# Performance work log

Measured on AMD Instinct MI355X. Metric: run time of the kernel, lower is better.

## Reference

```python
import jax, jax.numpy as jnp
import numpy as np

EMBED_DIM = 1024
EXPAND_RATIO = 128  # head_dim; n_heads = EMBED_DIM // EXPAND_RATIO = 8
B, N = 4, 2048


def setup_inputs() -> dict:
    key = jax.random.key(0)
    ks = jax.random.split(key, 6)
    std = 0.02
    d = EMBED_DIM
    return {
        "x": jax.random.normal(ks[0], (B, N, d), dtype=jnp.float32),
        "Wq": jax.random.normal(ks[1], (d, d), dtype=jnp.float32) * std,
        "Wk": jax.random.normal(ks[2], (d, d), dtype=jnp.float32) * std,
        "Wv": jax.random.normal(ks[3], (d, d), dtype=jnp.float32) * std,
        "Wo": jax.random.normal(ks[4], (d, d), dtype=jnp.float32) * std,
        "norm_w": jnp.ones((d,), dtype=jnp.float32),
    }


def _rmsnorm(x, w, eps=1e-6):
    return x * jax.lax.rsqrt(jnp.mean(x * x, axis=-1, keepdims=True) + eps) * w


def _gla_scan(q, k, v, g):
    # q,k,v,g: [b, n, h, d]; state S: [b, h, d_k, d_v]
    b, n, h, d = q.shape
    qs, ks_, vs, gs = (jnp.moveaxis(t, 1, 0) for t in (q, k, v, g))  # [n,b,h,d]
    S0 = jnp.zeros((b, h, d, d), dtype=q.dtype)

    def step(S, inp):
        q_t, k_t, v_t, g_t = inp
        # S_t = diag(exp(g_t)) S_{t-1} + k_t^T v_t (gate on key dim)
        S = jnp.exp(g_t)[..., :, None] * S + k_t[..., :, None] * v_t[..., None, :]
        o_t = jnp.einsum('bhk,bhkv->bhv', q_t, S)
        return S, o_t

    _, outs = jax.lax.scan(step, S0, (qs, ks_, vs, gs))
    return jnp.moveaxis(outs, 0, 1)  # [b, n, h, d]


def reference(x, Wq, Wk, Wv, Wo, norm_w):
    b, n, D = x.shape
    hd = EXPAND_RATIO
    h = D // hd

    q = jax.nn.silu(x @ Wq.T)          # q_activation = silu
    f = jax.nn.sigmoid(x @ Wk.T)       # f = sigmoid(k_proj(x))
    log_f = jax.nn.log_sigmoid(f)      # faithful: logsigmoid applied to f (lower_bound=None path)
    k = 1.0 - f
    v = x @ Wv.T

    def split_heads(t):
        return t.reshape(b, n, h, hd)

    out = _gla_scan(split_heads(q), split_heads(k), split_heads(v), split_heads(log_f))
    out = out.reshape(b, n, D)
    out = _rmsnorm(out, norm_w)        # norm_pos='ogate', no output gate
    return out @ Wo.T
```

## Files before the change

kernel.cpp:

```cpp
#include <hip/hip_runtime.h>
#include <cstdint>
#include <cstddef>


typedef unsigned short u16;
using f32x4  = __attribute__((ext_vector_type(4))) float;
using bf16x8 = __attribute__((ext_vector_type(8))) short;

__device__ __forceinline__ float bf2f(u16 u) {
  union { unsigned int i; float f; } v; v.i = ((unsigned int)u) << 16; return v.f;
}
__device__ __forceinline__ u16 f2bf(float f) {
  union { float f; unsigned int i; } v; v.f = f;
  unsigned int r = v.i + 0x7fffu + ((v.i >> 16) & 1u);
  return (u16)(r >> 16);
}
__device__ __forceinline__ void async_load16(const void* g, void* l) {
  __builtin_amdgcn_global_load_lds(
      (const __attribute__((address_space(1))) unsigned int*)(uintptr_t)g,
      (__attribute__((address_space(3))) unsigned int*)(uintptr_t)l, 16, 0, 0);
}

__device__ __forceinline__ void gemm128_core(const u16* __restrict__ Ag, const u16* __restrict__ Bg,
                                             u16* smem, f32x4 (&acc)[4][4]) {
  const int tid = threadIdx.x;
  const int lane = tid & 63, wave = tid >> 6;
  const int wm = (wave & 1) * 64, wn = (wave >> 1) * 64;
  const int r = lane & 15, quad = lane >> 4;
  const int xk = r & 7;
  const u16* baseA0 = smem + (wm + r) * 64 + ((quad ^ xk) & 7) * 8;
  const u16* baseA1 = smem + (wm + r) * 64 + (((quad + 4) ^ xk) & 7) * 8;
  const u16* baseB0 = smem + 8192 + (wn + r) * 64 + ((quad ^ xk) & 7) * 8;
  const u16* baseB1 = smem + 8192 + (wn + r) * 64 + (((quad + 4) ^ xk) & 7) * 8;
  const int soff = (tid >> 3) * 1024 + (((tid & 7) ^ ((tid >> 3) & 7)) * 8);
  u16* dA = smem + wave * 512;
  u16* dB = smem + 8192 + wave * 512;
  for (int kt = 0; kt < 16; ++kt) {
    __syncthreads();
    const u16* As = Ag + kt * 64 + soff;
    const u16* Bs = Bg + kt * 64 + soff;
#pragma unroll
    for (int it = 0; it < 4; ++it) {
      async_load16(As + it * 32768, dA + it * 2048);
      async_load16(Bs + it * 32768, dB + it * 2048);
    }
    __syncthreads();
    bf16x8 af[4], bv[4];
#pragma unroll
    for (int i = 0; i < 4; ++i) af[i] = *(const bf16x8*)(baseA0 + i * 1024);
#pragma unroll
    for (int j = 0; j < 4; ++j) bv[j] = *(const bf16x8*)(baseB0 + j * 1024);
#pragma unroll
    for (int i = 0; i < 4; ++i)
#pragma unroll
      for (int j = 0; j < 4; ++j)
        acc[i][j] = __builtin_amdgcn_mfma_f32_16x16x32_bf16(af[i], bv[j], acc[i][j], 0, 0, 0);
#pragma unroll
    for (int i = 0; i < 4; ++i) af[i] = *(const bf16x8*)(baseA1 + i * 1024);
#pragma unroll
    for (int j = 0; j < 4; ++j) bv[j] = *(const bf16x8*)(baseB1 + j * 1024);
#pragma unroll
    for (int i = 0; i < 4; ++i)
#pragma unroll
      for (int j = 0; j < 4; ++j)
        acc[i][j] = __builtin_amdgcn_mfma_f32_16x16x32_bf16(af[i], bv[j], acc[i][j], 0, 0, 0);
  }
}

__global__ __launch_bounds__(256) void cast_f32_bf16(const float* __restrict__ src,
                                                     u16* __restrict__ dst, int n4) {
  int i = blockIdx.x * 256 + threadIdx.x;
  if (i >= n4) return;
  float4 v = ((const float4*)src)[i];
  unsigned int lo = (unsigned)f2bf(v.x) | ((unsigned)f2bf(v.y) << 16);
  unsigned int hi = (unsigned)f2bf(v.z) | ((unsigned)f2bf(v.w) << 16);
  ((uint2*)dst)[i] = make_uint2(lo, hi);
}

__global__ __launch_bounds__(256) void cast_w4(const float* __restrict__ w0, const float* __restrict__ w1,
                                               const float* __restrict__ w2, const float* __restrict__ w3,
                                               u16* __restrict__ d0, u16* __restrict__ d1,
                                               u16* __restrict__ d2, u16* __restrict__ d3) {
  const float* src = blockIdx.y == 0 ? w0 : (blockIdx.y == 1 ? w1 : (blockIdx.y == 2 ? w2 : w3));
  u16* dst = blockIdx.y == 0 ? d0 : (blockIdx.y == 1 ? d1 : (blockIdx.y == 2 ? d2 : d3));
  int i = blockIdx.x * 256 + threadIdx.x;
  float4 v = ((const float4*)src)[i];
  unsigned int lo = (unsigned)f2bf(v.x) | ((unsigned)f2bf(v.y) << 16);
  unsigned int hi = (unsigned)f2bf(v.z) | ((unsigned)f2bf(v.w) << 16);
  ((uint2*)dst)[i] = make_uint2(lo, hi);
}

__global__ __launch_bounds__(256) void hgru_gemm_qkv(
    const u16* __restrict__ Xb, const u16* __restrict__ Wqb, const u16* __restrict__ Wkb,
    const u16* __restrict__ Wvb, u16* __restrict__ Qb, u16* __restrict__ Kb,
    u16* __restrict__ Vb) {
  __shared__ alignas(16) u16 smem[16384];
  const int which = blockIdx.y >> 3, bn = blockIdx.y & 7;
  const u16* W = which == 0 ? Wqb : (which == 1 ? Wkb : Wvb);
  const u16* Ag = Xb + (size_t)blockIdx.x * 128 * 1024;
  const u16* Bg = W + (size_t)bn * 128 * 1024;
  f32x4 acc[4][4] = {};
  gemm128_core(Ag, Bg, smem, acc);
  const int tid = threadIdx.x, lane = tid & 63, wave = tid >> 6;
  const int wm = (wave & 1) * 64, wn = (wave >> 1) * 64;
  const int r = lane & 15, quad = lane >> 4;
#pragma unroll
  for (int i = 0; i < 4; ++i)
#pragma unroll
    for (int j = 0; j < 4; ++j)
#pragma unroll
      for (int reg = 0; reg < 4; ++reg) {
        int m = blockIdx.x * 128 + wm + i * 16 + quad * 4 + reg;
        int n = bn * 128 + wn + j * 16 + r;
        size_t off = (size_t)m * 1024 + n;
        float z = acc[i][j][reg];
        if (which == 0) {
          Qb[off] = f2bf(z / (1.f + __expf(-z)));
        } else if (which == 1) {
          float ek = __expf(-z);
          Kb[off] = f2bf(ek / (1.f + ek));
        } else {
          Vb[off] = f2bf(z);
        }
      }
}

__global__ __launch_bounds__(256) void hgru_phaseA(
    u16* __restrict__ Qb, u16* __restrict__ Kb, const u16* __restrict__ Vb,
    u16* __restrict__ SU) {
  __shared__ alignas(16) float sb[64 * 129];
  __shared__ float sD[128];
  __shared__ alignas(16) u16 sKt[128 * 72];
  __shared__ alignas(16) u16 sVt[128 * 72];
  const int tid = threadIdx.x, blk = blockIdx.x;
  const int c = blk & 31, bh = blk >> 5, h = bh & 7, b = bh >> 3;
  const size_t rowbase = (size_t)(b * 2048 + c * 64) * 1024 + h * 128;

  {
    const int col = tid & 127, half = tid >> 7;
    const size_t gb = rowbase + (size_t)(half * 32) * 1024 + col;
    float run = 0.f;
#pragma unroll
    for (int t = 0; t < 32; ++t) {
      float kv = bf2f(Kb[gb + (size_t)t * 1024]);
      float f = 1.f - kv;
      run -= __logf(1.f + __expf(-f));
      sb[(half * 32 + t) * 129 + col] = run;
    }
  }
  __syncthreads();
  {
    const int col = tid & 127;
    if (tid >> 7) {
      float fix = sb[31 * 129 + col];
#pragma unroll
      for (int t = 32; t < 64; ++t) sb[t * 129 + col] += fix;
    }
  }
  __syncthreads();
  if (tid < 128) sD[tid] = __expf(sb[63 * 129 + tid]);
  __syncthreads();
#pragma unroll
  for (int kq = 0; kq < 4; ++kq) {
    int idx = kq * 256 + tid;
    int s = idx & 63, i8 = idx >> 6;
    size_t off = rowbase + (size_t)s * 1024 + i8 * 8;
    uint4 qr = *(const uint4*)(Qb + off);
    uint4 kr = *(const uint4*)(Kb + off);
    uint4 vr = *(const uint4*)(Vb + off);
    const u16* qp = (const u16*)&qr;
    const u16* kp = (const u16*)&kr;
    const u16* vp = (const u16*)&vr;
    u16 qo[8], ko[8];
#pragma unroll
    for (int e = 0; e < 8; ++e) {
      int i = i8 * 8 + e;
      float bb = sb[s * 129 + i];
      float ep = __expf(bb), en = __expf(-bb);
      float ktil = bf2f(kp[e]) * en;
      qo[e] = f2bf(bf2f(qp[e]) * ep);
      ko[e] = f2bf(ktil);
      sKt[i * 72 + s] = f2bf(ktil * sD[i]);
      sVt[i * 72 + s] = vp[e];
    }
    *(uint4*)(Qb + off) = *(const uint4*)qo;
    *(uint4*)(Kb + off) = *(const uint4*)ko;
  }
  __syncthreads();
  const int lane = tid & 63, wave = tid >> 6;
  const int wm = (wave & 1) * 64, wn = (wave >> 1) * 64;
  const int r = lane & 15, quad = lane >> 4;
  f32x4 acc[4][4] = {};
#pragma unroll
  for (int ks = 0; ks < 2; ++ks) {
    bf16x8 af[4], bv[4];
#pragma unroll
    for (int i = 0; i < 4; ++i) af[i] = *(const bf16x8*)(sVt + (wm + i * 16 + r) * 72 + ks * 32 + quad * 8);
#pragma unroll
    for (int j = 0; j < 4; ++j) bv[j] = *(const bf16x8*)(sKt + (wn + j * 16 + r) * 72 + ks * 32 + quad * 8);
#pragma unroll
    for (int i = 0; i < 4; ++i)
#pragma unroll
      for (int j = 0; j < 4; ++j)
        acc[i][j] = __builtin_amdgcn_mfma_f32_16x16x32_bf16(af[i], bv[j], acc[i][j], 0, 0, 0);
  }
  u16* SUo = SU + (size_t)blk * 16384;
#pragma unroll
  for (int i = 0; i < 4; ++i)
#pragma unroll
    for (int j = 0; j < 4; ++j)
#pragma unroll
      for (int reg = 0; reg < 4; ++reg) {
        int v = wm + i * 16 + quad * 4 + reg;
        int ii = wn + j * 16 + r;
        SUo[v * 128 + ii] = f2bf(acc[i][j][reg]);
      }
}

__global__ __launch_bounds__(256) void hgru_phaseC(
    const u16* __restrict__ Qh, const u16* __restrict__ Kt, const u16* __restrict__ Vb,
    const u16* __restrict__ SU, u16* __restrict__ O) {
  __shared__ alignas(16) u16 sQ[64 * 136];
  __shared__ alignas(16) u16 sK[64 * 136];
  __shared__ alignas(16) u16 sVt[128 * 72];
  __shared__ alignas(16) u16 sAm[64 * 72];
  const int tid = threadIdx.x, blk = blockIdx.x;
  const int c = blk & 31, bh = blk >> 5, h = bh & 7, b = bh >> 3;
  const size_t rowbase = (size_t)(b * 2048 + c * 64) * 1024 + h * 128;

#pragma unroll
  for (int kq = 0; kq < 4; ++kq) {
    int idx = kq * 256 + tid;
    int t = idx >> 4, j8 = idx & 15;
    size_t off = rowbase + (size_t)t * 1024 + j8 * 8;
    *(uint4*)(sQ + t * 136 + j8 * 8) = *(const uint4*)(Qh + off);
    *(uint4*)(sK + t * 136 + j8 * 8) = *(const uint4*)(Kt + off);
  }
#pragma unroll
  for (int kq = 0; kq < 4; ++kq) {
    int idx = kq * 256 + tid;
    int t = idx & 63, v8 = idx >> 6;
    uint4 vr = *(const uint4*)(Vb + rowbase + (size_t)t * 1024 + v8 * 8);
    const u16* vp = (const u16*)&vr;
#pragma unroll
    for (int e = 0; e < 8; ++e) sVt[(v8 * 8 + e) * 72 + t] = vp[e];
  }
  __syncthreads();
  const int lane = tid & 63, wave = tid >> 6;
  const int r = lane & 15, quad = lane >> 4;
  {
    f32x4 a1[4] = {};
#pragma unroll
    for (int ks = 0; ks < 4; ++ks) {
      bf16x8 af = *(const bf16x8*)(sQ + (wave * 16 + r) * 136 + ks * 32 + quad * 8);
#pragma unroll
      for (int nj = 0; nj < 4; ++nj) {
        bf16x8 bk = *(const bf16x8*)(sK + (nj * 16 + r) * 136 + ks * 32 + quad * 8);
        a1[nj] = __builtin_amdgcn_mfma_f32_16x16x32_bf16(af, bk, a1[nj], 0, 0, 0);
      }
    }
#pragma unroll
    for (int nj = 0; nj < 4; ++nj)
#pragma unroll
      for (int reg = 0; reg < 4; ++reg) {
        int t = wave * 16 + quad * 4 + reg;
        int s = nj * 16 + r;
        sAm[t * 72 + s] = (s <= t) ? f2bf(a1[nj][reg]) : (u16)0;
      }
  }
  const u16* U1 = SU + (size_t)(bh * 32 + (c - 1)) * 16384;
  const bool haveS = (c >= 1);
#pragma unroll
  for (int j = 0; j < 8; ++j) {
    f32x4 acc2 = {0.f, 0.f, 0.f, 0.f};
#pragma unroll
    for (int ks = 0; ks < 2; ++ks) {
      bf16x8 af = *(const bf16x8*)(sAm + (wave * 16 + r) * 72 + ks * 32 + quad * 8);
      bf16x8 bv = *(const bf16x8*)(sVt + (j * 16 + r) * 72 + ks * 32 + quad * 8);
      acc2 = __builtin_amdgcn_mfma_f32_16x16x32_bf16(af, bv, acc2, 0, 0, 0);
    }
    if (haveS) {
#pragma unroll
      for (int ks = 0; ks < 4; ++ks) {
        bf16x8 afq = *(const bf16x8*)(sQ + (wave * 16 + r) * 136 + ks * 32 + quad * 8);
        bf16x8 bs = *(const bf16x8*)(U1 + (j * 16 + r) * 128 + ks * 32 + quad * 8);
        acc2 = __builtin_amdgcn_mfma_f32_16x16x32_bf16(afq, bs, acc2, 0, 0, 0);
      }
    }
#pragma unroll
    for (int reg = 0; reg < 4; ++reg) {
      int t = wave * 16 + quad * 4 + reg;
      int v = j * 16 + r;
      O[rowbase + (size_t)t * 1024 + v] = f2bf(acc2[reg]);
    }
  }
}

__global__ __launch_bounds__(256) void hgru_rmsnorm(const u16* __restrict__ O,
                                                    const float* __restrict__ w,
                                                    u16* __restrict__ On) {
  __shared__ float sred[4];
  const int row = blockIdx.x, tid = threadIdx.x;
  const size_t base = (size_t)row * 1024;
  float vals[4];
  float ss = 0.f;
#pragma unroll
  for (int k = 0; k < 4; ++k) {
    float v = bf2f(O[base + k * 256 + tid]);
    vals[k] = v;
    ss += v * v;
  }
#pragma unroll
  for (int m = 32; m >= 1; m >>= 1) ss += __shfl_xor(ss, m);
  if ((tid & 63) == 0) sred[tid >> 6] = ss;
  __syncthreads();
  float tot = sred[0] + sred[1] + sred[2] + sred[3];
  float scale = rsqrtf(tot * (1.f / 1024.f) + 1e-6f);
#pragma unroll
  for (int k = 0; k < 4; ++k)
    On[base + k * 256 + tid] = f2bf(vals[k] * scale * w[k * 256 + tid]);
}

__global__ __launch_bounds__(256) void hgru_gemm_out(const u16* __restrict__ Ab,
                                                     const u16* __restrict__ Wob,
                                                     float* __restrict__ out) {
  __shared__ alignas(16) u16 smem[16384];
  const u16* Ag = Ab + (size_t)blockIdx.x * 128 * 1024;
  const u16* Bg = Wob + (size_t)blockIdx.y * 128 * 1024;
  f32x4 acc[4][4] = {};
  gemm128_core(Ag, Bg, smem, acc);
  const int tid = threadIdx.x, lane = tid & 63, wave = tid >> 6;
  const int wm = (wave & 1) * 64, wn = (wave >> 1) * 64;
  const int r = lane & 15, quad = lane >> 4;
#pragma unroll
  for (int i = 0; i < 4; ++i)
#pragma unroll
    for (int j = 0; j < 4; ++j)
#pragma unroll
      for (int reg = 0; reg < 4; ++reg) {
        int m = blockIdx.x * 128 + wm + i * 16 + quad * 4 + reg;
        int n = blockIdx.y * 128 + wn + j * 16 + r;
        out[(size_t)m * 1024 + n] = acc[i][j][reg];
      }
}

extern "C" void kernel_launch(void* const* d_in, const int* in_sizes, int n_in,
                              void* d_out, int out_size, void* d_ws, size_t ws_size,
                              hipStream_t stream) {
  const float* x  = (const float*)d_in[0];
  const float* Wq = (const float*)d_in[1];
  const float* Wk = (const float*)d_in[2];
  const float* Wv = (const float*)d_in[3];
  const float* Wo = (const float*)d_in[4];
  const float* nw = (const float*)d_in[5];
  float* out = (float*)d_out;
  char* ws = (char*)d_ws;

  u16* Xb   = (u16*)(ws + 0);
  u16* Wqb  = (u16*)(ws + 16777216);
  u16* Wkb  = (u16*)(ws + 18874368);
  u16* Wvb  = (u16*)(ws + 20971520);
  u16* Wob  = (u16*)(ws + 23068672);
  u16* Qb   = (u16*)(ws + 25165824);
  u16* Kb   = (u16*)(ws + 41943040);
  u16* Vb   = (u16*)(ws + 58720256);
  u16* SU   = (u16*)(ws + 75497472);
  u16* Obf  = (u16*)(ws + 109051904);
  u16* On   = Xb;

  cast_f32_bf16<<<8192, 256, 0, stream>>>(x, Xb, 2097152);
  dim3 gw(1024, 4);
  cast_w4<<<gw, 256, 0, stream>>>(Wq, Wk, Wv, Wo, Wqb, Wkb, Wvb, Wob);

  dim3 gq(64, 24);
  hgru_gemm_qkv<<<gq, 256, 0, stream>>>(Xb, Wqb, Wkb, Wvb, Qb, Kb, Vb);
  hgru_phaseA<<<1024, 256, 0, stream>>>(Qb, Kb, Vb, SU);
  hgru_phaseC<<<1024, 256, 0, stream>>>(Qb, Kb, Vb, SU, Obf);
  hgru_rmsnorm<<<8192, 256, 0, stream>>>(Obf, nw, On);
  dim3 go(64, 8);
  hgru_gemm_out<<<go, 256, 0, stream>>>(On, Wob, out);
}
```

Measured before the change: 261.0 us.

## Fuse chunk-state and output phases into one scan kernel with local state recompute

Replaces the two-kernel chunked scan (one kernel writes per-chunk states to global memory, a second reads them) with a single kernel. Chunks shrink to 32 steps and the value dimension is split across two blocks. Each block recomputes the previous chunk's decayed state contribution in shared memory, so the large state buffer is never written to or read back from global memory, and one launch goes away. The cost is redundant gate cumsum and state work in every block. It also keeps only one previous chunk of history, which relies on the bounded per-step decay; with 32-step chunks that window is now shorter than before.

```diff
diff --git a/kernel.cpp b/kernel.cpp
--- a/kernel.cpp
+++ b/kernel.cpp
@@ -125,175 +125,171 @@
       }
 }
 
-__global__ __launch_bounds__(256) void hgru_phaseA(
-    u16* __restrict__ Qb, u16* __restrict__ Kb, const u16* __restrict__ Vb,
-    u16* __restrict__ SU) {
-  __shared__ alignas(16) float sb[64 * 129];
-  __shared__ float sD[128];
-  __shared__ alignas(16) u16 sKt[128 * 72];
-  __shared__ alignas(16) u16 sVt[128 * 72];
+__global__ __launch_bounds__(256) void hgru_scan(
+    const u16* __restrict__ Qg, const u16* __restrict__ Kg, const u16* __restrict__ Vg,
+    u16* __restrict__ O) {
+  __shared__ alignas(16) char smem[59008];
+  float* sb = (float*)(smem);
+  u16* sU   = (u16*)(smem + 16512);
+  u16* sKt  = (u16*)(smem + 33920);
+  u16* sVt1 = (u16*)(smem + 44160);
+  u16* sQ   = (u16*)(smem + 33920);
+  u16* sK   = (u16*)(smem + 42624);
+  u16* sAm  = (u16*)(smem + 51328);
+  u16* sVt2 = (u16*)(smem + 53888);
+
   const int tid = threadIdx.x, blk = blockIdx.x;
-  const int c = blk & 31, bh = blk >> 5, h = bh & 7, b = bh >> 3;
-  const size_t rowbase = (size_t)(b * 2048 + c * 64) * 1024 + h * 128;
-
-  {
-    const int col = tid & 127, half = tid >> 7;
-    const size_t gb = rowbase + (size_t)(half * 32) * 1024 + col;
+  const int vh = blk & 1, c = (blk >> 1) & 63, bh = blk >> 7, h = bh & 7, bb_ = bh >> 3;
+  const size_t rb = (size_t)(bb_ * 2048 + c * 32) * 1024 + h * 128;
+  const bool haveP = (c > 0);
+  const size_t rb1 = haveP ? rb - 32 * 1024 : rb;
+
+  const int lane = tid & 63, wave = tid >> 6;
+  const int r = lane & 15, quad = lane >> 4;
+  const int ts = tid & 31;
+  const int g8 = tid >> 5;
+
+  uint4 Q2[2], K2[2], K1[2], V2, V1;
+#pragma unroll
+  for (int it = 0; it < 2; ++it) {
+    Q2[it] = *(const uint4*)(Qg + rb  + (size_t)ts * 1024 + (it * 8 + g8) * 8);
+    K2[it] = *(const uint4*)(Kg + rb  + (size_t)ts * 1024 + (it * 8 + g8) * 8);
+    K1[it] = *(const uint4*)(Kg + rb1 + (size_t)ts * 1024 + (it * 8 + g8) * 8);
+  }
+  V2 = *(const uint4*)(Vg + rb  + (size_t)ts * 1024 + vh * 64 + g8 * 8);
+  V1 = *(const uint4*)(Vg + rb1 + (size_t)ts * 1024 + vh * 64 + g8 * 8);
+
+  f32x4 accU[2][4] = {};
+  const int vm = (wave & 1) * 32, in = (wave >> 1) * 64;
+
+  if (haveP) {
+    { const int col = tid & 127, half = tid >> 7;
+      float run = 0.f;
+      const size_t gb = rb1 + (size_t)(half * 16) * 1024 + col;
+#pragma unroll
+      for (int t = 0; t < 16; ++t) {
+        float kv = bf2f(Kg[gb + (size_t)t * 1024]);
+        run -= __logf(1.f + __expf(-(1.f - kv)));
+        sb[(half * 16 + t) * 129 + col] = run;
+      } }
+    __syncthreads();
+    { if (tid >> 7) { const int col = tid & 127; float fix = sb[15 * 129 + col];
+#pragma unroll
+        for (int t = 16; t < 32; ++t) sb[t * 129 + col] += fix; } }
+    __syncthreads();
+#pragma unroll
+    for (int it = 0; it < 2; ++it) {
+      const int i8 = it * 8 + g8;
+      const u16* kp = (const u16*)&K1[it];
+#pragma unroll
+      for (int e = 0; e < 8; ++e) {
+        int i = i8 * 8 + e;
+        float bs = sb[ts * 129 + i];
+        float bC = sb[31 * 129 + i];
+        sKt[i * 40 + ts] = f2bf(bf2f(kp[e]) * __expf(bC - bs));
+      }
+    }
+    { const u16* vp = (const u16*)&V1;
+#pragma unroll
+      for (int e = 0; e < 8; ++e) sVt1[(g8 * 8 + e) * 40 + ts] = vp[e]; }
+    __syncthreads();
+#pragma unroll
+    for (int mi = 0; mi < 2; ++mi) {
+      bf16x8 af = *(const bf16x8*)(sVt1 + (vm + mi * 16 + r) * 40 + quad * 8);
+#pragma unroll
+      for (int nj = 0; nj < 4; ++nj) {
+        bf16x8 bv = *(const bf16x8*)(sKt + (in + nj * 16 + r) * 40 + quad * 8);
+        accU[mi][nj] = __builtin_amdgcn_mfma_f32_16x16x32_bf16(af, bv, accU[mi][nj], 0, 0, 0);
+      }
+    }
+  }
+  { const int col = tid & 127, half = tid >> 7;
     float run = 0.f;
-#pragma unroll
-    for (int t = 0; t < 32; ++t) {
-      float kv = bf2f(Kb[gb + (size_t)t * 1024]);
-      float f = 1.f - kv;
-      run -= __logf(1.f + __expf(-f));
-      sb[(half * 32 + t) * 129 + col] = run;
-    }
-  }
-  __syncthreads();
-  {
-    const int col = tid & 127;
-    if (tid >> 7) {
-      float fix = sb[31 * 129 + col];
-#pragma unroll
-      for (int t = 32; t < 64; ++t) sb[t * 129 + col] += fix;
-    }
-  }
-  __syncthreads();
-  if (tid < 128) sD[tid] = __expf(sb[63 * 129 + tid]);
-  __syncthreads();
-#pragma unroll
-  for (int kq = 0; kq < 4; ++kq) {
-    int idx = kq * 256 + tid;
-    int s = idx & 63, i8 = idx >> 6;
-    size_t off = rowbase + (size_t)s * 1024 + i8 * 8;
-    uint4 qr = *(const uint4*)(Qb + off);
-    uint4 kr = *(const uint4*)(Kb + off);
-    uint4 vr = *(const uint4*)(Vb + off);
-    const u16* qp = (const u16*)&qr;
-    const u16* kp = (const u16*)&kr;
-    const u16* vp = (const u16*)&vr;
+    const size_t gb = rb + (size_t)(half * 16) * 1024 + col;
+#pragma unroll
+    for (int t = 0; t < 16; ++t) {
+      float kv = bf2f(Kg[gb + (size_t)t * 1024]);
+      run -= __logf(1.f + __expf(-(1.f - kv)));
+      sb[(half * 16 + t) * 129 + col] = run;
+    } }
+  __syncthreads();
+  { if (tid >> 7) { const int col = tid & 127; float fix = sb[15 * 129 + col];
+#pragma unroll
+      for (int t = 16; t < 32; ++t) sb[t * 129 + col] += fix; } }
+  if (haveP) {
+#pragma unroll
+    for (int mi = 0; mi < 2; ++mi)
+#pragma unroll
+      for (int nj = 0; nj < 4; ++nj)
+#pragma unroll
+        for (int reg = 0; reg < 4; ++reg) {
+          int vl = vm + mi * 16 + quad * 4 + reg;
+          int i  = in + nj * 16 + r;
+          sU[vl * 136 + i] = f2bf(accU[mi][nj][reg]);
+        }
+  }
+  __syncthreads();
+#pragma unroll
+  for (int it = 0; it < 2; ++it) {
+    const int i8 = it * 8 + g8;
+    const u16* qp = (const u16*)&Q2[it];
+    const u16* kp = (const u16*)&K2[it];
     u16 qo[8], ko[8];
 #pragma unroll
     for (int e = 0; e < 8; ++e) {
       int i = i8 * 8 + e;
-      float bb = sb[s * 129 + i];
-      float ep = __expf(bb), en = __expf(-bb);
-      float ktil = bf2f(kp[e]) * en;
-      qo[e] = f2bf(bf2f(qp[e]) * ep);
-      ko[e] = f2bf(ktil);
-      sKt[i * 72 + s] = f2bf(ktil * sD[i]);
-      sVt[i * 72 + s] = vp[e];
-    }
-    *(uint4*)(Qb + off) = *(const uint4*)qo;
-    *(uint4*)(Kb + off) = *(const uint4*)ko;
-  }
-  __syncthreads();
-  const int lane = tid & 63, wave = tid >> 6;
-  const int wm = (wave & 1) * 64, wn = (wave >> 1) * 64;
-  const int r = lane & 15, quad = lane >> 4;
-  f32x4 acc[4][4] = {};
-#pragma unroll
-  for (int ks = 0; ks < 2; ++ks) {
-    bf16x8 af[4], bv[4];
-#pragma unroll
-    for (int i = 0; i < 4; ++i) af[i] = *(const bf16x8*)(sVt + (wm + i * 16 + r) * 72 + ks * 32 + quad * 8);
-#pragma unroll
-    for (int j = 0; j < 4; ++j) bv[j] = *(const bf16x8*)(sKt + (wn + j * 16 + r) * 72 + ks * 32 + quad * 8);
-#pragma unroll
-    for (int i = 0; i < 4; ++i)
-#pragma unroll
-      for (int j = 0; j < 4; ++j)
-        acc[i][j] = __builtin_amdgcn_mfma_f32_16x16x32_bf16(af[i], bv[j], acc[i][j], 0, 0, 0);
-  }
-  u16* SUo = SU + (size_t)blk * 16384;
-#pragma unroll
-  for (int i = 0; i < 4; ++i)
-#pragma unroll
-    for (int j = 0; j < 4; ++j)
+      float bt = sb[ts * 129 + i];
+      qo[e] = f2bf(bf2f(qp[e]) * __expf(bt));
+      ko[e] = f2bf(bf2f(kp[e]) * __expf(-bt));
+    }
+    *(uint4*)(sQ + ts * 136 + i8 * 8) = *(const uint4*)qo;
+    *(uint4*)(sK + ts * 136 + i8 * 8) = *(const uint4*)ko;
+  }
+  { const u16* vp = (const u16*)&V2;
+#pragma unroll
+    for (int e = 0; e < 8; ++e) sVt2[(g8 * 8 + e) * 40 + ts] = vp[e]; }
+  __syncthreads();
+  { const int mi = wave & 1, nj = wave >> 1;
+    f32x4 a1 = {0.f, 0.f, 0.f, 0.f};
+#pragma unroll
+    for (int ks = 0; ks < 4; ++ks) {
+      bf16x8 af = *(const bf16x8*)(sQ + (mi * 16 + r) * 136 + ks * 32 + quad * 8);
+      bf16x8 bk = *(const bf16x8*)(sK + (nj * 16 + r) * 136 + ks * 32 + quad * 8);
+      a1 = __builtin_amdgcn_mfma_f32_16x16x32_bf16(af, bk, a1, 0, 0, 0);
+    }
+#pragma unroll
+    for (int reg = 0; reg < 4; ++reg) {
+      int t = mi * 16 + quad * 4 + reg, s = nj * 16 + r;
+      sAm[t * 40 + s] = (s <= t) ? f2bf(a1[reg]) : (u16)0;
+    } }
+  __syncthreads();
+  { const int mi = wave & 1, no = (wave >> 1) * 32;
+    bf16x8 af0 = *(const bf16x8*)(sAm + (mi * 16 + r) * 40 + quad * 8);
+    bf16x8 afq[4];
+    if (haveP) {
+#pragma unroll
+      for (int ks = 0; ks < 4; ++ks)
+        afq[ks] = *(const bf16x8*)(sQ + (mi * 16 + r) * 136 + ks * 32 + quad * 8);
+    }
+#pragma unroll
+    for (int j = 0; j < 2; ++j) {
+      f32x4 acc2 = {0.f, 0.f, 0.f, 0.f};
+      bf16x8 bv0 = *(const bf16x8*)(sVt2 + (no + j * 16 + r) * 40 + quad * 8);
+      acc2 = __builtin_amdgcn_mfma_f32_16x16x32_bf16(af0, bv0, acc2, 0, 0, 0);
+      if (haveP) {
+#pragma unroll
+        for (int ks = 0; ks < 4; ++ks) {
+          bf16x8 bs = *(const bf16x8*)(sU + (no + j * 16 + r) * 136 + ks * 32 + quad * 8);
+          acc2 = __builtin_amdgcn_mfma_f32_16x16x32_bf16(afq[ks], bs, acc2, 0, 0, 0);
+        }
+      }
 #pragma unroll
       for (int reg = 0; reg < 4; ++reg) {
-        int v = wm + i * 16 + quad * 4 + reg;
-        int ii = wn + j * 16 + r;
-        SUo[v * 128 + ii] = f2bf(acc[i][j][reg]);
-      }
-}
-
-__global__ __launch_bounds__(256) void hgru_phaseC(
-    const u16* __restrict__ Qh, const u16* __restrict__ Kt, const u16* __restrict__ Vb,
-    const u16* __restrict__ SU, u16* __restrict__ O) {
-  __shared__ alignas(16) u16 sQ[64 * 136];
-  __shared__ alignas(16) u16 sK[64 * 136];
-  __shared__ alignas(16) u16 sVt[128 * 72];
-  __shared__ alignas(16) u16 sAm[64 * 72];
-  const int tid = threadIdx.x, blk = blockIdx.x;
-  const int c = blk & 31, bh = blk >> 5, h = bh & 7, b = bh >> 3;
-  const size_t rowbase = (size_t)(b * 2048 + c * 64) * 1024 + h * 128;
-
-#pragma unroll
-  for (int kq = 0; kq < 4; ++kq) {
-    int idx = kq * 256 + tid;
-    int t = idx >> 4, j8 = idx & 15;
-    size_t off = rowbase + (size_t)t * 1024 + j8 * 8;
-    *(uint4*)(sQ + t * 136 + j8 * 8) = *(const uint4*)(Qh + off);
-    *(uint4*)(sK + t * 136 + j8 * 8) = *(const uint4*)(Kt + off);
-  }
-#pragma unroll
-  for (int kq = 0; kq < 4; ++kq) {
-    int idx = kq * 256 + tid;
-    int t = idx & 63, v8 = idx >> 6;
-    uint4 vr = *(const uint4*)(Vb + rowbase + (size_t)t * 1024 + v8 * 8);
-    const u16* vp = (const u16*)&vr;
-#pragma unroll
-    for (int e = 0; e < 8; ++e) sVt[(v8 * 8 + e) * 72 + t] = vp[e];
-  }
-  __syncthreads();
-  const int lane = tid & 63, wave = tid >> 6;
-  const int r = lane & 15, quad = lane >> 4;
-  {
-    f32x4 a1[4] = {};
-#pragma unroll
-    for (int ks = 0; ks < 4; ++ks) {
-      bf16x8 af = *(const bf16x8*)(sQ + (wave * 16 + r) * 136 + ks * 32 + quad * 8);
-#pragma unroll
-      for (int nj = 0; nj < 4; ++nj) {
-        bf16x8 bk = *(const bf16x8*)(sK + (nj * 16 + r) * 136 + ks * 32 + quad * 8);
-        a1[nj] = __builtin_amdgcn_mfma_f32_16x16x32_bf16(af, bk, a1[nj], 0, 0, 0);
-      }
-    }
-#pragma unroll
-    for (int nj = 0; nj < 4; ++nj)
-#pragma unroll
-      for (int reg = 0; reg < 4; ++reg) {
-        int t = wave * 16 + quad * 4 + reg;
-        int s = nj * 16 + r;
-        sAm[t * 72 + s] = (s <= t) ? f2bf(a1[nj][reg]) : (u16)0;
-      }
-  }
-  const u16* U1 = SU + (size_t)(bh * 32 + (c - 1)) * 16384;
-  const bool haveS = (c >= 1);
-#pragma unroll
-  for (int j = 0; j < 8; ++j) {
-    f32x4 acc2 = {0.f, 0.f, 0.f, 0.f};
-#pragma unroll
-    for (int ks = 0; ks < 2; ++ks) {
-      bf16x8 af = *(const bf16x8*)(sAm + (wave * 16 + r) * 72 + ks * 32 + quad * 8);
-      bf16x8 bv = *(const bf16x8*)(sVt + (j * 16 + r) * 72 + ks * 32 + quad * 8);
-      acc2 = __builtin_amdgcn_mfma_f32_16x16x32_bf16(af, bv, acc2, 0, 0, 0);
-    }
-    if (haveS) {
-#pragma unroll
-      for (int ks = 0; ks < 4; ++ks) {
-        bf16x8 afq = *(const bf16x8*)(sQ + (wave * 16 + r) * 136 + ks * 32 + quad * 8);
-        bf16x8 bs = *(const bf16x8*)(U1 + (j * 16 + r) * 128 + ks * 32 + quad * 8);
-        acc2 = __builtin_amdgcn_mfma_f32_16x16x32_bf16(afq, bs, acc2, 0, 0, 0);
-      }
-    }
-#pragma unroll
-    for (int reg = 0; reg < 4; ++reg) {
-      int t = wave * 16 + quad * 4 + reg;
-      int v = j * 16 + r;
-      O[rowbase + (size_t)t * 1024 + v] = f2bf(acc2[reg]);
-    }
-  }
+        int t = mi * 16 + quad * 4 + reg;
+        int vg = vh * 64 + no + j * 16 + r;
+        O[rb + (size_t)t * 1024 + vg] = f2bf(acc2[reg]);
+      }
+    } }
 }
 
 __global__ __launch_bounds__(256) void hgru_rmsnorm(const u16* __restrict__ O,
@@ -364,8 +360,7 @@
   u16* Qb   = (u16*)(ws + 25165824);
   u16* Kb   = (u16*)(ws + 41943040);
   u16* Vb   = (u16*)(ws + 58720256);
-  u16* SU   = (u16*)(ws + 75497472);
-  u16* Obf  = (u16*)(ws + 109051904);
+  u16* Obf  = (u16*)(ws + 75497472);
   u16* On   = Xb;
 
   cast_f32_bf16<<<8192, 256, 0, stream>>>(x, Xb, 2097152);
@@ -374,8 +369,7 @@
 
   dim3 gq(64, 24);
   hgru_gemm_qkv<<<gq, 256, 0, stream>>>(Xb, Wqb, Wkb, Wvb, Qb, Kb, Vb);
-  hgru_phaseA<<<1024, 256, 0, stream>>>(Qb, Kb, Vb, SU);
-  hgru_phaseC<<<1024, 256, 0, stream>>>(Qb, Kb, Vb, SU, Obf);
+  hgru_scan<<<4096, 256, 0, stream>>>(Qb, Kb, Vb, Obf);
   hgru_rmsnorm<<<8192, 256, 0, stream>>>(Obf, nw, On);
   dim3 go(64, 8);
   hgru_gemm_out<<<go, 256, 0, stream>>>(On, Wob, out);
```

Result: no change. 263.1 us (+0.8%).
